# Kernel optimization log

Hardware: AMD Instinct MI355X
Metric: run time of the kernel (lower is better)

The kernel has to match this reference:

```python
import jax, jax.numpy as jnp
import numpy as np

B = 2; D = 256; NH = 8; NL = 4; HD = D // NH
K = 2; P = K * K; NV = 4; DFF = 1024
SHAPES = ((128, 128), (64, 64), (32, 32), (16, 16))
LV = sum(h * w for h, w in SHAPES)
START = np.cumsum([0] + [h * w for h, w in SHAPES])[:-1].tolist()
EPS = 1e-5

# fixed 2x2 sampling kernel, matching _create_kernel_indices (even kernel branch)
_ind = np.linspace(-0.5, 0.5, K)
_ii, _jj = np.meshgrid(_ind, _ind, indexing='ij')
KERNEL = jnp.asarray(np.stack([_jj, _ii], -1).reshape(-1, 2) / K, jnp.float32)  # (P,2)


def _layer_norm(x, w, b):
    m = x.mean(-1, keepdims=True)
    v = ((x - m) ** 2).mean(-1, keepdims=True)
    return (x - m) * jax.lax.rsqrt(v + EPS) * w + b


def _box_attention(query, value, ref_windows, vpw, vpb, opw, opb, boxw, boxb, attw, attb):
    b, lq, _ = query.shape
    # value projection, split into heads: (b, NH, LV, HD)
    v = (value @ vpw.T + vpb).reshape(b, LV, NH, HD).transpose(0, 2, 1, 3)

    # attention weights: softmax over all (level, point) jointly per head
    aw = query @ attw.T + attb
    aw = jax.nn.softmax(aw.reshape(b, lq, NH, NL * P), -1).reshape(b, lq, NH, NL, P)

    # where to attend (with_rotation=False -> 4 offset variables, angle from ref)
    ob = (query @ boxw.T + boxb).reshape(b, lq, NH, NL, NV)
    rw = ref_windows[:, :, None, None, :]                    # (b,lq,1,1,7)
    ref_boxes = rw[..., jnp.array([0, 1, 3, 4])]
    angles = jnp.broadcast_to(rw[..., 6:7], (b, lq, NH, NL, 1))
    boxes = ref_boxes + ob / 8.0 * ref_boxes[..., jnp.array([2, 3, 2, 3])]
    center = boxes[..., None, :2]                            # (b,lq,NH,NL,1,2)
    size = boxes[..., None, 2:]
    c, s = jnp.cos(angles), jnp.sin(angles)
    rot = jnp.stack([c, -s, s, c], -1).reshape(b, lq, NH, NL, 1, 2, 2)
    g = KERNEL * jax.nn.relu(size)                           # (b,lq,NH,NL,P,2)
    grid = center + (g[..., None, :] * rot).sum(-1)          # (b,lq,NH,NL,P,2)

    # multi-level bilinear sampling (= grid_sample align_corners=False, zero pad)
    bidx = jnp.arange(b)[:, None, None, None]
    hidx = jnp.arange(NH)[None, None, :, None]
    out = jnp.zeros((b, lq, NH, HD), v.dtype)
    for lvl, (H, W) in enumerate(SHAPES):
        st = START[lvl]
        vl = v[:, :, st:st + H * W]                          # (b,NH,HW,HD)
        loc = grid[:, :, :, lvl]                             # (b,lq,NH,P,2)
        x = loc[..., 0] * W - 0.5
        y = loc[..., 1] * H - 0.5
        x0f = jnp.floor(x); y0f = jnp.floor(y)
        wx = x - x0f; wy = y - y0f
        x0 = x0f.astype(jnp.int32); y0 = y0f.astype(jnp.int32)
        acc = jnp.zeros((b, lq, NH, P, HD), v.dtype)
        corners = ((0, 0, (1 - wx) * (1 - wy)), (1, 0, wx * (1 - wy)),
                   (0, 1, (1 - wx) * wy), (1, 1, wx * wy))
        for dx, dy, wgt in corners:
            xi = x0 + dx; yi = y0 + dy
            valid = (xi >= 0) & (xi < W) & (yi >= 0) & (yi < H)
            idx = jnp.clip(yi, 0, H - 1) * W + jnp.clip(xi, 0, W - 1)
            samp = vl[bidx, hidx, idx]                       # (b,lq,NH,P,HD)
            acc = acc + (wgt * valid)[..., None] * samp
        out = out + jnp.einsum('blhp,blhpd->blhd', aw[:, :, :, lvl], acc)
    return out.reshape(b, lq, D) @ opw.T + opb


def setup_inputs() -> dict:
    key = jax.random.key(0)
    ks = jax.random.split(key, 20)
    def nrm(k, shape, fan_in):
        return jax.random.normal(k, shape, jnp.float32) * (1.0 / np.sqrt(fan_in))
    rw = jax.random.uniform(ks[2], (B, LV, 7), jnp.float32)
    # keep window sizes (cols 3,4,5) modest, like real BEV reference windows
    rw = rw.at[..., 3:6].multiply(0.2)
    return {
        'src': jax.random.normal(ks[0], (B, LV, D), jnp.float32),
        'pos': jax.random.normal(ks[1], (B, LV, D), jnp.float32),
        'src_shape': jnp.asarray(SHAPES, jnp.int32),
        'src_start_idx': jnp.asarray(START, jnp.int32),
        'ref_windows': rw,
        'vpw': nrm(ks[3], (D, D), D), 'vpb': jnp.zeros((D,), jnp.float32),
        'opw': nrm(ks[4], (D, D), D), 'opb': jnp.zeros((D,), jnp.float32),
        'boxw': nrm(ks[5], (NL * NH * NV, D), D) * 0.1,
        'boxb': jax.random.normal(ks[6], (NL * NH * NV,), jnp.float32) * 0.1,
        'attw': nrm(ks[7], (NH * NL * P, D), D),
        'attb': jnp.zeros((NH * NL * P,), jnp.float32),
        'lin1_w': nrm(ks[8], (DFF, D), D), 'lin1_b': jnp.zeros((DFF,), jnp.float32),
        'lin2_w': nrm(ks[9], (D, DFF), DFF), 'lin2_b': jnp.zeros((D,), jnp.float32),
        'ln1_w': jnp.ones((D,), jnp.float32), 'ln1_b': jnp.zeros((D,), jnp.float32),
        'ln2_w': jnp.ones((D,), jnp.float32), 'ln2_b': jnp.zeros((D,), jnp.float32),
    }


def reference(src, pos, src_shape, src_start_idx, ref_windows,
              vpw, vpb, opw, opb, boxw, boxb, attw, attb,
              lin1_w, lin1_b, lin2_w, lin2_b, ln1_w, ln1_b, ln2_w, ln2_b):
    # level shapes/starts are static (SHAPES/START constants); src_shape /
    # src_start_idx are accepted for signature fidelity.
    src2 = _box_attention(src + pos, src, ref_windows,
                          vpw, vpb, opw, opb, boxw, boxb, attw, attb)
    src = _layer_norm(src + src2, ln1_w, ln1_b)
    ffn = jax.nn.relu(src @ lin1_w.T + lin1_b) @ lin2_w.T + lin2_b
    return _layer_norm(src + ffn, ln2_w, ln2_b)
```

## Files before the change

kernel.cpp:

```cpp
#include <hip/hip_runtime.h>
#include <stdint.h>

typedef unsigned short u16;
typedef __attribute__((ext_vector_type(8))) short short8;
typedef __attribute__((ext_vector_type(4))) float f32x4;

#define D_    256
#define NH_   8
#define HD_   32
#define LV_   21760
#define DFF_  1024
#define EPS_  1e-5f
#define MH_   21760
#define MT_   43520

__device__ __forceinline__ float bf2f(u16 u) {
    union { uint32_t i; float f; } x; x.i = ((uint32_t)u) << 16; return x.f;
}
__device__ __forceinline__ u16 f2bf(float f) {
    union { float f; uint32_t i; } x; x.f = f;
    uint32_t r = x.i + 0x7FFFu + ((x.i >> 16) & 1u);
    return (u16)(r >> 16);
}
__device__ __forceinline__ uint32_t pk2(float a, float b) {
    return (uint32_t)f2bf(a) | ((uint32_t)f2bf(b) << 16);
}
__device__ __forceinline__ float blo(uint32_t u) {
    union { uint32_t i; float f; } x; x.i = u << 16; return x.f;
}
__device__ __forceinline__ float bhi(uint32_t u) {
    union { uint32_t i; float f; } x; x.i = u & 0xffff0000u; return x.f;
}
__device__ __forceinline__ void cv8(u16* dst, float4 a, float4 b) {
    uint4 r;
    r.x = pk2(a.x, a.y); r.y = pk2(a.z, a.w);
    r.z = pk2(b.x, b.y); r.w = pk2(b.z, b.w);
    *(uint4*)dst = r;
}
__device__ __forceinline__ void cv8add(u16* dst, float4 a, float4 a2, float4 b, float4 b2) {
    uint4 r;
    r.x = pk2(a.x + a2.x, a.y + a2.y); r.y = pk2(a.z + a2.z, a.w + a2.w);
    r.z = pk2(b.x + b2.x, b.y + b2.y); r.w = pk2(b.z + b2.z, b.w + b2.w);
    *(uint4*)dst = r;
}

__global__ __launch_bounds__(256) void k_cvt(const float* __restrict__ in,
                                             u16* __restrict__ out, int n4) {
    int i = blockIdx.x * 256 + threadIdx.x;
    if (i < n4) {
        float4 v = ((const float4*)in)[i];
        uint2 r; r.x = pk2(v.x, v.y); r.y = pk2(v.z, v.w);
        *(uint2*)(out + (size_t)i * 4) = r;
    }
}

__global__ __launch_bounds__(256) void k_vprojm(
        const float* __restrict__ src, const float* __restrict__ vpw,
        const float* __restrict__ vpb, u16* __restrict__ vout) {
    __shared__ u16 As[2][64 * 32];
    __shared__ u16 Bs[2][64 * 32];
    const int t = threadIdx.x;
    const int l = t & 63, w = t >> 6;
    const int m0 = blockIdx.x * 64, n0 = blockIdx.y * 64;
    const int sr = t >> 2, sc = t & 3;
    const int wslot = sr * 32 + ((sc ^ ((sr >> 1) & 3)) << 3);
    const float* gA = src + (size_t)(m0 + sr) * 256 + sc * 8;
    const float* gB = vpw + (size_t)(n0 + sr) * 256 + sc * 8;
    const int fr = l & 15, fg = l >> 4;
    const int wm = w >> 1, wn = w & 1;

    f32x4 acc[2][2];
    #pragma unroll
    for (int mi = 0; mi < 2; ++mi)
        #pragma unroll
        for (int ni = 0; ni < 2; ++ni)
            acc[mi][ni] = (f32x4){0.f, 0.f, 0.f, 0.f};

    cv8(&As[0][wslot], *(const float4*)gA, *(const float4*)(gA + 4));
    cv8(&Bs[0][wslot], *(const float4*)gB, *(const float4*)(gB + 4));
    __syncthreads();

    for (int kt = 0; kt < 8; ++kt) {
        const int cur = kt & 1;
        float4 na0, na1, nb0, nb1;
        if (kt < 7) {
            na0 = *(const float4*)(gA + (kt + 1) * 32);
            na1 = *(const float4*)(gA + (kt + 1) * 32 + 4);
            nb0 = *(const float4*)(gB + (kt + 1) * 32);
            nb1 = *(const float4*)(gB + (kt + 1) * 32 + 4);
        }
        short8 af[2], bfr[2];
        #pragma unroll
        for (int mi = 0; mi < 2; ++mi) {
            const int r = wm * 32 + mi * 16 + fr;
            af[mi] = *(const short8*)&As[cur][r * 32 + ((fg ^ ((r >> 1) & 3)) << 3)];
        }
        #pragma unroll
        for (int ni = 0; ni < 2; ++ni) {
            const int r = wn * 32 + ni * 16 + fr;
            bfr[ni] = *(const short8*)&Bs[cur][r * 32 + ((fg ^ ((r >> 1) & 3)) << 3)];
        }
        #pragma unroll
        for (int mi = 0; mi < 2; ++mi)
            #pragma unroll
            for (int ni = 0; ni < 2; ++ni)
                acc[mi][ni] = __builtin_amdgcn_mfma_f32_16x16x32_bf16(af[mi], bfr[ni], acc[mi][ni], 0, 0, 0);
        if (kt < 7) {
            cv8(&As[cur ^ 1][wslot], na0, na1);
            cv8(&Bs[cur ^ 1][wslot], nb0, nb1);
            __syncthreads();
        }
    }
    const int b = m0 / LV_;
    #pragma unroll
    for (int ni = 0; ni < 2; ++ni) {
        const int n = n0 + wn * 32 + ni * 16 + fr;
        const float bv = vpb[n];
        const int h = n >> 5, hd = n & 31;
        #pragma unroll
        for (int mi = 0; mi < 2; ++mi) {
            #pragma unroll
            for (int q = 0; q < 4; ++q) {
                const int m = m0 + wm * 32 + mi * 16 + fg * 4 + q;
                const int lrow = m - b * LV_;
                vout[((size_t)(b * NH_ + h) * LV_ + lrow) * HD_ + hd] = f2bf(acc[mi][ni][q] + bv);
            }
        }
    }
}

__global__ __launch_bounds__(256) void k_logits(
        const float* __restrict__ src, const float* __restrict__ pos,
        const float* __restrict__ attw, const float* __restrict__ attb,
        const float* __restrict__ boxw, const float* __restrict__ boxb,
        u16* __restrict__ lgout) {
    __shared__ u16 As[2][64 * 32];
    __shared__ u16 Bs[2][64 * 32];
    const int t = threadIdx.x;
    const int l = t & 63, w = t >> 6;
    const int m0 = blockIdx.x * 64;
    const int n0g = blockIdx.y * 64;
    const float* Bsrc = (n0g < 128) ? (attw + (size_t)n0g * 256) : (boxw + (size_t)(n0g - 128) * 256);
    const float* bsrc = (n0g < 128) ? (attb + n0g) : (boxb + (n0g - 128));
    const int sr = t >> 2, sc = t & 3;
    const int wslot = sr * 32 + ((sc ^ ((sr >> 1) & 3)) << 3);
    const float* gAs = src + (size_t)(m0 + sr) * 256 + sc * 8;
    const float* gAp = pos + (size_t)(m0 + sr) * 256 + sc * 8;
    const float* gB  = Bsrc + (size_t)sr * 256 + sc * 8;
    const int fr = l & 15, fg = l >> 4;
    const int wm = w >> 1, wn = w & 1;

    f32x4 acc[2][2];
    #pragma unroll
    for (int mi = 0; mi < 2; ++mi)
        #pragma unroll
        for (int ni = 0; ni < 2; ++ni)
            acc[mi][ni] = (f32x4){0.f, 0.f, 0.f, 0.f};

    cv8add(&As[0][wslot], *(const float4*)gAs, *(const float4*)gAp,
                          *(const float4*)(gAs + 4), *(const float4*)(gAp + 4));
    cv8(&Bs[0][wslot], *(const float4*)gB, *(const float4*)(gB + 4));
    __syncthreads();

    for (int kt = 0; kt < 8; ++kt) {
        const int cur = kt & 1;
        float4 ns0, ns1, np0, np1, nb0, nb1;
        if (kt < 7) {
            ns0 = *(const float4*)(gAs + (kt + 1) * 32);
            ns1 = *(const float4*)(gAs + (kt + 1) * 32 + 4);
            np0 = *(const float4*)(gAp + (kt + 1) * 32);
            np1 = *(const float4*)(gAp + (kt + 1) * 32 + 4);
            nb0 = *(const float4*)(gB + (kt + 1) * 32);
            nb1 = *(const float4*)(gB + (kt + 1) * 32 + 4);
        }
        short8 af[2], bfr[2];
        #pragma unroll
        for (int mi = 0; mi < 2; ++mi) {
            const int r = wm * 32 + mi * 16 + fr;
            af[mi] = *(const short8*)&As[cur][r * 32 + ((fg ^ ((r >> 1) & 3)) << 3)];
        }
        #pragma unroll
        for (int ni = 0; ni < 2; ++ni) {
            const int r = wn * 32 + ni * 16 + fr;
            bfr[ni] = *(const short8*)&Bs[cur][r * 32 + ((fg ^ ((r >> 1) & 3)) << 3)];
        }
        #pragma unroll
        for (int mi = 0; mi < 2; ++mi)
            #pragma unroll
            for (int ni = 0; ni < 2; ++ni)
                acc[mi][ni] = __builtin_amdgcn_mfma_f32_16x16x32_bf16(af[mi], bfr[ni], acc[mi][ni], 0, 0, 0);
        if (kt < 7) {
            cv8add(&As[cur ^ 1][wslot], ns0, np0, ns1, np1);
            cv8(&Bs[cur ^ 1][wslot], nb0, nb1);
            __syncthreads();
        }
    }
    #pragma unroll
    for (int ni = 0; ni < 2; ++ni) {
        const int nl_ = wn * 32 + ni * 16 + fr;
        const int n = n0g + nl_;
        const float bv = bsrc[nl_];
        const int off = (n < 128) ? ((n >> 4) * 32 + (n & 15))
                                  : (((n - 128) >> 4) * 32 + 16 + ((n - 128) & 15));
        #pragma unroll
        for (int mi = 0; mi < 2; ++mi) {
            #pragma unroll
            for (int q = 0; q < 4; ++q) {
                const int m = m0 + wm * 32 + mi * 16 + fg * 4 + q;
                lgout[(size_t)m * 256 + off] = f2bf(acc[mi][ni][q] + bv);
            }
        }
    }
}

__global__ __launch_bounds__(256) void k_sample(
        const u16* __restrict__ lg, const float* __restrict__ refw,
        const u16* __restrict__ vws, u16* __restrict__ smp) {
    __shared__ float LG[16][2][32];
    __shared__ float RW[16][8];
    __shared__ __align__(16) uint2 CWI[32 * 66];
    const int t = threadIdx.x;
    const int bid = blockIdx.x;
    const int combo = bid & 7;
    const int idx = bid >> 3;
    const int b = combo >> 2, hp = combo & 3;
    const int h0 = hp * 2;
    const long gr0 = (long)b * LV_ + (long)idx * 16;

    {
        const int row = t >> 4, part = t & 15;
        const uint2 v = *(const uint2*)(lg + (size_t)(gr0 + row) * 256 + h0 * 32 + part * 4);
        const int hs = part >> 3, kk = (part & 7) * 4;
        LG[row][hs][kk]     = blo(v.x);
        LG[row][hs][kk + 1] = bhi(v.x);
        LG[row][hs][kk + 2] = blo(v.y);
        LG[row][hs][kk + 3] = bhi(v.y);
        if (t < 112) {
            int r2 = t / 7, k = t % 7;
            RW[r2][k] = refw[(gr0 + r2) * 7 + k];
        }
    }
    __syncthreads();
    if (t < 32) {
        const int row = t >> 1, hs = t & 1;
        float* a = LG[row][hs];
        float m = a[0];
        #pragma unroll
        for (int k = 1; k < 16; ++k) m = fmaxf(m, a[k]);
        float s = 0.f;
        float e[16];
        #pragma unroll
        for (int k = 0; k < 16; ++k) { e[k] = __expf(a[k] - m); s += e[k]; }
        const float inv = 1.f / s;
        #pragma unroll
        for (int k = 0; k < 16; ++k) a[k] = e[k] * inv;
    }
    __syncthreads();
    #pragma unroll
    for (int uu = 0; uu < 2; ++uu) {
        const int u = t + uu * 256;
        const int row = u >> 5, rem = u & 31;
        const int hs = rem >> 4, nl = (rem >> 2) & 3, p = rem & 3;
        const float rw0 = RW[row][0], rw1 = RW[row][1], rw3 = RW[row][3], rw4 = RW[row][4], ang = RW[row][6];
        const float ob0 = LG[row][hs][16 + nl * 4 + 0];
        const float ob1 = LG[row][hs][16 + nl * 4 + 1];
        const float ob2 = LG[row][hs][16 + nl * 4 + 2];
        const float ob3 = LG[row][hs][16 + nl * 4 + 3];
        const float cx = rw0 + ob0 * 0.125f * rw3;
        const float cy = rw1 + ob1 * 0.125f * rw4;
        const float bw = fmaxf(rw3 + ob2 * 0.125f * rw3, 0.f);
        const float bh = fmaxf(rw4 + ob3 * 0.125f * rw4, 0.f);
        const float kx = (p & 1) ? 0.25f : -0.25f;
        const float ky = (p >> 1) ? 0.25f : -0.25f;
        float sth, cth;
        __sincosf(ang, &sth, &cth);
        const float g0 = kx * bw, g1 = ky * bh;
        const float gx = cx + g0 * cth - g1 * sth;
        const float gy = cy + g0 * sth + g1 * cth;
        const int Wl = 128 >> nl;
        const int st = (65536 - (65536 >> (2 * nl))) / 3;
        const float x = gx * Wl - 0.5f, y = gy * Wl - 0.5f;
        const float xf = floorf(x), yf = floorf(y);
        const float wx = x - xf, wy = y - yf;
        const int x0 = (int)xf, y0 = (int)yf;
        const float awv = LG[row][hs][nl * 4 + p];
        uint2 cw[4];
        #pragma unroll
        for (int c4 = 0; c4 < 4; ++c4) {
            const int dx = c4 & 1, dy = c4 >> 1;
            const int xi = x0 + dx, yi = y0 + dy;
            const float wgt = (dx ? wx : 1.f - wx) * (dy ? wy : 1.f - wy);
            const bool valid = (xi >= 0) && (xi < Wl) && (yi >= 0) && (yi < Wl);
            const int xc = xi < 0 ? 0 : (xi > Wl - 1 ? Wl - 1 : xi);
            const int yc = yi < 0 ? 0 : (yi > Wl - 1 ? Wl - 1 : yi);
            const float wv = valid ? wgt * awv : 0.f;
            cw[c4].x = __float_as_uint(wv);
            cw[c4].y = (uint32_t)(st + yc * Wl + xc) * 64u;
        }
        uint2* dst = &CWI[(row * 2 + hs) * 66 + (nl * 4 + p) * 4];
        *(uint4*)(dst)     = *(const uint4*)&cw[0];
        *(uint4*)(dst + 2) = *(const uint4*)&cw[2];
    }
    __syncthreads();
    {
        const int e = t & 7, g = t >> 3;
        const int row = g >> 1, hs = g & 1, h = h0 + hs;
        const char* vbp = (const char*)vws +
            (((size_t)(b * NH_ + h) * LV_) * HD_ + e * 4) * 2;
        const uint2* cbase = &CWI[g * 66];
        float a0 = 0.f, a1 = 0.f, a2 = 0.f, a3 = 0.f;
        #pragma unroll 4
        for (int k = 0; k < 16; ++k) {
            #pragma unroll
            for (int cc = 0; cc < 2; ++cc) {
                const uint4 cw2 = *(const uint4*)&cbase[k * 4 + cc * 2];
                const float w0 = __uint_as_float(cw2.x);
                const uint2 d0 = *(const uint2*)(vbp + cw2.y);
                const float w1 = __uint_as_float(cw2.z);
                const uint2 d1 = *(const uint2*)(vbp + cw2.w);
                a0 += w0 * blo(d0.x); a1 += w0 * bhi(d0.x);
                a2 += w0 * blo(d0.y); a3 += w0 * bhi(d0.y);
                a0 += w1 * blo(d1.x); a1 += w1 * bhi(d1.x);
                a2 += w1 * blo(d1.y); a3 += w1 * bhi(d1.y);
            }
        }
        uint2 o; o.x = pk2(a0, a1); o.y = pk2(a2, a3);
        *(uint2*)(smp + (size_t)(gr0 + row) * 256 + h * 32 + e * 4) = o;
    }
}

__global__ __launch_bounds__(256) void k_oproj(
        const u16* __restrict__ A,
        const float* __restrict__ opw,
        const float* __restrict__ opb,
        const float* __restrict__ src,
        const float* __restrict__ lnw, const float* __restrict__ lnb,
        u16* __restrict__ out) {
    __shared__ char smem[36864];
    u16* As = (u16*)smem;
    u16* Bs = (u16*)(smem + 4096);
    float* Y = (float*)smem;
    const int t = threadIdx.x;
    const int l = t & 63, w = t >> 6;
    const int m0 = blockIdx.x * 32;
    const int sAr = t >> 2, sc = t & 3;
    const int aslot = sAr * 32 + ((sc ^ ((sAr >> 1) & 3)) << 3);
    const u16* gA = A + (size_t)(m0 + sAr) * 256 + sc * 8;
    const float* gB[4];
    int bslot[4];
    #pragma unroll
    for (int i = 0; i < 4; ++i) {
        const int r = (t >> 2) + i * 64;
        gB[i] = opw + (size_t)r * 256 + sc * 8;
        bslot[i] = r * 32 + ((sc ^ ((r >> 1) & 3)) << 3);
    }
    const int fr = l & 15, fg = l >> 4;

    f32x4 acc[2][4];
    #pragma unroll
    for (int mi = 0; mi < 2; ++mi)
        #pragma unroll
        for (int ni = 0; ni < 4; ++ni)
            acc[mi][ni] = (f32x4){0.f, 0.f, 0.f, 0.f};

    if (t < 128) *(uint4*)&As[aslot] = *(const uint4*)gA;
    #pragma unroll
    for (int i = 0; i < 4; ++i)
        cv8(&Bs[bslot[i]], *(const float4*)gB[i], *(const float4*)(gB[i] + 4));
    __syncthreads();

    for (int kt = 0; kt < 8; ++kt) {
        const int cur = kt & 1;
        uint4 na; float4 nb[4][2];
        if (kt < 7) {
            if (t < 128) na = *(const uint4*)(gA + (kt + 1) * 32);
            #pragma unroll
            for (int i = 0; i < 4; ++i) {
                nb[i][0] = *(const float4*)(gB[i] + (kt + 1) * 32);
                nb[i][1] = *(const float4*)(gB[i] + (kt + 1) * 32 + 4);
            }
        }
        short8 af[2], bfr[4];
        #pragma unroll
        for (int mi = 0; mi < 2; ++mi) {
            const int r = mi * 16 + fr;
            af[mi] = *(const short8*)&As[cur * 1024 + r * 32 + ((fg ^ ((r >> 1) & 3)) << 3)];
        }
        #pragma unroll
        for (int ni = 0; ni < 4; ++ni) {
            const int r = w * 64 + ni * 16 + fr;
            bfr[ni] = *(const short8*)&Bs[cur * 8192 + r * 32 + ((fg ^ ((r >> 1) & 3)) << 3)];
        }
        #pragma unroll
        for (int mi = 0; mi < 2; ++mi)
            #pragma unroll
            for (int ni = 0; ni < 4; ++ni)
                acc[mi][ni] = __builtin_amdgcn_mfma_f32_16x16x32_bf16(af[mi], bfr[ni], acc[mi][ni], 0, 0, 0);
        if (kt < 7) {
            if (t < 128) *(uint4*)&As[(cur ^ 1) * 1024 + aslot] = na;
            #pragma unroll
            for (int i = 0; i < 4; ++i)
                cv8(&Bs[(cur ^ 1) * 8192 + bslot[i]], nb[i][0], nb[i][1]);
            __syncthreads();
        }
    }
    __syncthreads();
    #pragma unroll
    for (int ni = 0; ni < 4; ++ni) {
        const int n = w * 64 + ni * 16 + fr;
        const float bv = opb[n];
        #pragma unroll
        for (int mi = 0; mi < 2; ++mi) {
            #pragma unroll
            for (int q = 0; q < 4; ++q) {
                const int ml = mi * 16 + fg * 4 + q;
                Y[ml * 256 + n] = acc[mi][ni][q] + bv + src[(size_t)(m0 + ml) * 256 + n];
            }
        }
    }
    __syncthreads();
    for (int rr = 0; rr < 8; ++rr) {
        const int m = w * 8 + rr;
        const float v0 = Y[m * 256 + l];
        const float v1 = Y[m * 256 + 64 + l];
        const float v2 = Y[m * 256 + 128 + l];
        const float v3 = Y[m * 256 + 192 + l];
        float s1 = v0 + v1 + v2 + v3;
        float s2 = v0 * v0 + v1 * v1 + v2 * v2 + v3 * v3;
        #pragma unroll
        for (int off = 32; off; off >>= 1) {
            s1 += __shfl_xor(s1, off);
            s2 += __shfl_xor(s2, off);
        }
        const float mean = s1 * (1.f / 256.f);
        const float var = s2 * (1.f / 256.f) - mean * mean;
        const float rs = rsqrtf(var + EPS_);
        const size_t ob = (size_t)(m0 + m) * 256;
        out[ob + l]       = f2bf((v0 - mean) * rs * lnw[l]       + lnb[l]);
        out[ob + 64 + l]  = f2bf((v1 - mean) * rs * lnw[64 + l]  + lnb[64 + l]);
        out[ob + 128 + l] = f2bf((v2 - mean) * rs * lnw[128 + l] + lnb[128 + l]);
        out[ob + 192 + l] = f2bf((v3 - mean) * rs * lnw[192 + l] + lnb[192 + l]);
    }
}

__global__ __launch_bounds__(256) void k_gemm1(
        const u16* __restrict__ A, const u16* __restrict__ Bw,
        const float* __restrict__ bias, u16* __restrict__ H) {
    __shared__ u16 As[2][128 * 32];
    __shared__ u16 Bs[2][128 * 32];
    const int t = threadIdx.x;
    const int l = t & 63, w = t >> 6;
    const int m0 = blockIdx.x * 128, n0 = blockIdx.y * 128;
    const int sr = t >> 1, sc0 = (t & 1) * 2;
    const int ws0 = sr * 32 + ((sc0 ^ ((sr >> 1) & 3)) << 3);
    const int ws1 = sr * 32 + (((sc0 + 1) ^ ((sr >> 1) & 3)) << 3);
    const u16* gA = A + (size_t)(m0 + sr) * 256 + sc0 * 8;
    const u16* gB = Bw + (size_t)(n0 + sr) * 256 + sc0 * 8;
    const int fr = l & 15, fg = l >> 4;
    const int wm = w >> 1, wn = w & 1;

    f32x4 acc[4][4];
    #pragma unroll
    for (int mi = 0; mi < 4; ++mi)
        #pragma unroll
        for (int ni = 0; ni < 4; ++ni)
            acc[mi][ni] = (f32x4){0.f, 0.f, 0.f, 0.f};

    *(uint4*)&As[0][ws0] = *(const uint4*)(gA);
    *(uint4*)&As[0][ws1] = *(const uint4*)(gA + 8);
    *(uint4*)&Bs[0][ws0] = *(const uint4*)(gB);
    *(uint4*)&Bs[0][ws1] = *(const uint4*)(gB + 8);
    __syncthreads();

    for (int kt = 0; kt < 8; ++kt) {
        const int cur = kt & 1;
        uint4 na0, na1, nb0, nb1;
        if (kt < 7) {
            na0 = *(const uint4*)(gA + (kt + 1) * 32);
            na1 = *(const uint4*)(gA + (kt + 1) * 32 + 8);
            nb0 = *(const uint4*)(gB + (kt + 1) * 32);
            nb1 = *(const uint4*)(gB + (kt + 1) * 32 + 8);
        }
        short8 af[4], bfr[4];
        #pragma unroll
        for (int mi = 0; mi < 4; ++mi) {
            const int r = wm * 64 + mi * 16 + fr;
            af[mi] = *(const short8*)&As[cur][r * 32 + ((fg ^ ((r >> 1) & 3)) << 3)];
        }
        #pragma unroll
        for (int ni = 0; ni < 4; ++ni) {
            const int r = wn * 64 + ni * 16 + fr;
            bfr[ni] = *(const short8*)&Bs[cur][r * 32 + ((fg ^ ((r >> 1) & 3)) << 3)];
        }
        #pragma unroll
        for (int mi = 0; mi < 4; ++mi)
            #pragma unroll
            for (int ni = 0; ni < 4; ++ni)
                acc[mi][ni] = __builtin_amdgcn_mfma_f32_16x16x32_bf16(af[mi], bfr[ni], acc[mi][ni], 0, 0, 0);
        if (kt < 7) {
            *(uint4*)&As[cur ^ 1][ws0] = na0;
            *(uint4*)&As[cur ^ 1][ws1] = na1;
            *(uint4*)&Bs[cur ^ 1][ws0] = nb0;
            *(uint4*)&Bs[cur ^ 1][ws1] = nb1;
            __syncthreads();
        }
    }
    #pragma unroll
    for (int ni = 0; ni < 4; ++ni) {
        const int n = n0 + wn * 64 + ni * 16 + fr;
        const float bv = bias[n];
        #pragma unroll
        for (int mi = 0; mi < 4; ++mi) {
            #pragma unroll
            for (int q = 0; q < 4; ++q) {
                const int m = m0 + wm * 64 + mi * 16 + fg * 4 + q;
                const float v = acc[mi][ni][q] + bv;
                H[(size_t)m * 1024 + n] = f2bf(fmaxf(v, 0.f));
            }
        }
    }
}

__global__ __launch_bounds__(256) void k_gemm2(
        const u16* __restrict__ A, const u16* __restrict__ Bw,
        const float* __restrict__ bias, const u16* __restrict__ resid,
        const float* __restrict__ lnw, const float* __restrict__ lnb,
        float* __restrict__ out) {
    __shared__ char smem[36864];
    u16* As = (u16*)smem;
    u16* Bs = (u16*)(smem + 4096);
    float* Y = (float*)smem;
    const int t = threadIdx.x;
    const int l = t & 63, w = t >> 6;
    const int m0 = blockIdx.x * 32;
    const int sAr = t >> 2, sc = t & 3;
    const int aslot = sAr * 32 + ((sc ^ ((sAr >> 1) & 3)) << 3);
    const u16* gA = A + (size_t)(m0 + sAr) * 1024 + sc * 8;
    const u16* gB[4];
    int bslot[4];
    #pragma unroll
    for (int i = 0; i < 4; ++i) {
        const int r = (t >> 2) + i * 64;
        gB[i] = Bw + (size_t)r * 1024 + sc * 8;
        bslot[i] = r * 32 + ((sc ^ ((r >> 1) & 3)) << 3);
    }
    const int fr = l & 15, fg = l >> 4;

    f32x4 acc[2][4];
    #pragma unroll
    for (int mi = 0; mi < 2; ++mi)
        #pragma unroll
        for (int ni = 0; ni < 4; ++ni)
            acc[mi][ni] = (f32x4){0.f, 0.f, 0.f, 0.f};

    if (t < 128) *(uint4*)&As[aslot] = *(const uint4*)(gA);
    #pragma unroll
    for (int i = 0; i < 4; ++i) *(uint4*)&Bs[bslot[i]] = *(const uint4*)(gB[i]);
    __syncthreads();

    for (int kt = 0; kt < 32; ++kt) {
        const int cur = kt & 1;
        uint4 na, nb[4];
        if (kt < 31) {
            if (t < 128) na = *(const uint4*)(gA + (kt + 1) * 32);
            #pragma unroll
            for (int i = 0; i < 4; ++i) nb[i] = *(const uint4*)(gB[i] + (kt + 1) * 32);
        }
        short8 af[2], bfr[4];
        #pragma unroll
        for (int mi = 0; mi < 2; ++mi) {
            const int r = mi * 16 + fr;
            af[mi] = *(const short8*)&As[cur * 1024 + r * 32 + ((fg ^ ((r >> 1) & 3)) << 3)];
        }
        #pragma unroll
        for (int ni = 0; ni < 4; ++ni) {
            const int r = w * 64 + ni * 16 + fr;
            bfr[ni] = *(const short8*)&Bs[cur * 8192 + r * 32 + ((fg ^ ((r >> 1) & 3)) << 3)];
        }
        #pragma unroll
        for (int mi = 0; mi < 2; ++mi)
            #pragma unroll
            for (int ni = 0; ni < 4; ++ni)
                acc[mi][ni] = __builtin_amdgcn_mfma_f32_16x16x32_bf16(af[mi], bfr[ni], acc[mi][ni], 0, 0, 0);
        if (kt < 31) {
            if (t < 128) *(uint4*)&As[(cur ^ 1) * 1024 + aslot] = na;
            #pragma unroll
            for (int i = 0; i < 4; ++i) *(uint4*)&Bs[(cur ^ 1) * 8192 + bslot[i]] = nb[i];
            __syncthreads();
        }
    }
    __syncthreads();
    #pragma unroll
    for (int ni = 0; ni < 4; ++ni) {
        const int n = w * 64 + ni * 16 + fr;
        const float bv = bias[n];
        #pragma unroll
        for (int mi = 0; mi < 2; ++mi) {
            #pragma unroll
            for (int q = 0; q < 4; ++q) {
                const int ml = mi * 16 + fg * 4 + q;
                Y[ml * 256 + n] = acc[mi][ni][q] + bv + bf2f(resid[(size_t)(m0 + ml) * 256 + n]);
            }
        }
    }
    __syncthreads();
    for (int rr = 0; rr < 8; ++rr) {
        const int m = w * 8 + rr;
        const float v0 = Y[m * 256 + l];
        const float v1 = Y[m * 256 + 64 + l];
        const float v2 = Y[m * 256 + 128 + l];
        const float v3 = Y[m * 256 + 192 + l];
        float s1 = v0 + v1 + v2 + v3;
        float s2 = v0 * v0 + v1 * v1 + v2 * v2 + v3 * v3;
        #pragma unroll
        for (int off = 32; off; off >>= 1) {
            s1 += __shfl_xor(s1, off);
            s2 += __shfl_xor(s2, off);
        }
        const float mean = s1 * (1.f / 256.f);
        const float var = s2 * (1.f / 256.f) - mean * mean;
        const float rs = rsqrtf(var + EPS_);
        const size_t ob = (size_t)(m0 + m) * 256;
        out[ob + l]        = (v0 - mean) * rs * lnw[l]        + lnb[l];
        out[ob + 64 + l]   = (v1 - mean) * rs * lnw[64 + l]   + lnb[64 + l];
        out[ob + 128 + l]  = (v2 - mean) * rs * lnw[128 + l]  + lnb[128 + l];
        out[ob + 192 + l]  = (v3 - mean) * rs * lnw[192 + l]  + lnb[192 + l];
    }
}

extern "C" void kernel_launch(void* const* d_in, const int* in_sizes, int n_in,
                              void* d_out, int out_size, void* d_ws, size_t ws_size,
                              hipStream_t stream) {
    const float* src  = (const float*)d_in[0];
    const float* pos  = (const float*)d_in[1];
    const float* refw = (const float*)d_in[4];
    const float* vpw  = (const float*)d_in[5];
    const float* vpb  = (const float*)d_in[6];
    const float* opw  = (const float*)d_in[7];
    const float* opb  = (const float*)d_in[8];
    const float* boxw = (const float*)d_in[9];
    const float* boxb = (const float*)d_in[10];
    const float* attw = (const float*)d_in[11];
    const float* attb = (const float*)d_in[12];
    const float* l1w  = (const float*)d_in[13];
    const float* l1b  = (const float*)d_in[14];
    const float* l2w  = (const float*)d_in[15];
    const float* l2b  = (const float*)d_in[16];
    const float* ln1w = (const float*)d_in[17];
    const float* ln1b = (const float*)d_in[18];
    const float* ln2w = (const float*)d_in[19];
    const float* ln2b = (const float*)d_in[20];

    u16*   vws    = (u16*)d_ws;
    u16*   l1wb   = (u16*)d_ws;
    u16*   l2wb   = (u16*)((char*)d_ws + 524288);
    u16*   logitsb= (u16*)((char*)d_ws + 22282240u);
    u16*   src1b  = (u16*)((char*)d_ws + 22282240u);
    u16*   Hbf    = (u16*)((char*)d_ws + 44564480u);
    u16*   smp    = (u16*)((char*)d_ws + 66846720u);

    hipLaunchKernelGGL(k_vprojm, dim3(680, 4), dim3(256), 0, stream, src, vpw, vpb, vws);
    hipLaunchKernelGGL(k_logits, dim3(680, 4), dim3(256), 0, stream,
                       src, pos, attw, attb, boxw, boxb, logitsb);
    hipLaunchKernelGGL(k_sample, dim3(10880), dim3(256), 0, stream, logitsb, refw, vws, smp);
    hipLaunchKernelGGL(k_cvt, dim3(256), dim3(256), 0, stream, l1w, l1wb, 65536);
    hipLaunchKernelGGL(k_cvt, dim3(256), dim3(256), 0, stream, l2w, l2wb, 65536);
    hipLaunchKernelGGL(k_oproj, dim3(1360), dim3(256), 0, stream,
                       smp, opw, opb, src, ln1w, ln1b, src1b);
    for (int h = 0; h < 2; ++h) {
        const u16* Ah = src1b + (size_t)h * MH_ * 256;
        float* outh   = (float*)d_out + (size_t)h * MH_ * 256;
        hipLaunchKernelGGL(k_gemm1, dim3(170, 8), dim3(256), 0, stream, Ah, l1wb, l1b, Hbf);
        hipLaunchKernelGGL(k_gemm2, dim3(680), dim3(256), 0, stream, Hbf, l2wb, l2b, Ah, ln2w, ln2b, outh);
    }
}
```

Baseline: 320.8 us.

## Double M tiles in projection GEMMs, use hardware bf16 pack, repad sampler LDS

Doubles the M tile of k_vprojm and k_logits to 128 rows and of k_oproj to 64 rows, so each weight tile loaded from global memory and converted is reused across more rows and fewer blocks are launched. Replaces the software round-to-nearest bf16 packing with the v_cvt_pk_bf16_f32 instruction. Changes the k_sample LDS layout with new padding and a precomputed head-plane offset to reduce bank conflicts and address math. k_oproj now stages the pre-LayerNorm residual in LDS as bf16 rather than fp32 to fit the larger tile, which adds rounding before the normalisation statistics and raises register pressure.

```diff
diff --git a/kernel.cpp b/kernel.cpp
--- a/kernel.cpp
+++ b/kernel.cpp
@@ -17,13 +17,13 @@
 __device__ __forceinline__ float bf2f(u16 u) {
     union { uint32_t i; float f; } x; x.i = ((uint32_t)u) << 16; return x.f;
 }
+__device__ __forceinline__ uint32_t pk2(float a, float b) {
+    uint32_t r;
+    asm("v_cvt_pk_bf16_f32 %0, %1, %2" : "=v"(r) : "v"(a), "v"(b));
+    return r;
+}
 __device__ __forceinline__ u16 f2bf(float f) {
-    union { float f; uint32_t i; } x; x.f = f;
-    uint32_t r = x.i + 0x7FFFu + ((x.i >> 16) & 1u);
-    return (u16)(r >> 16);
-}
-__device__ __forceinline__ uint32_t pk2(float a, float b) {
-    return (uint32_t)f2bf(a) | ((uint32_t)f2bf(b) << 16);
+    return (u16)(pk2(f, f) & 0xffffu);
 }
 __device__ __forceinline__ float blo(uint32_t u) {
     union { uint32_t i; float f; } x; x.i = u << 16; return x.f;
@@ -57,42 +57,48 @@
 __global__ __launch_bounds__(256) void k_vprojm(
         const float* __restrict__ src, const float* __restrict__ vpw,
         const float* __restrict__ vpb, u16* __restrict__ vout) {
-    __shared__ u16 As[2][64 * 32];
+    __shared__ u16 As[2][128 * 32];
     __shared__ u16 Bs[2][64 * 32];
     const int t = threadIdx.x;
     const int l = t & 63, w = t >> 6;
-    const int m0 = blockIdx.x * 64, n0 = blockIdx.y * 64;
-    const int sr = t >> 2, sc = t & 3;
-    const int wslot = sr * 32 + ((sc ^ ((sr >> 1) & 3)) << 3);
-    const float* gA = src + (size_t)(m0 + sr) * 256 + sc * 8;
-    const float* gB = vpw + (size_t)(n0 + sr) * 256 + sc * 8;
+    const int m0 = blockIdx.x * 128, n0 = blockIdx.y * 64;
+    const int r0 = t >> 2, c0 = t & 3;
+    const int wsA0 = r0 * 32 + ((c0 ^ ((r0 >> 1) & 3)) << 3);
+    const int wsA1 = wsA0 + 64 * 32;
+    const int wsB  = wsA0;
+    const float* gA0 = src + (size_t)(m0 + r0) * 256 + c0 * 8;
+    const float* gA1 = gA0 + (size_t)64 * 256;
+    const float* gB  = vpw + (size_t)(n0 + r0) * 256 + c0 * 8;
     const int fr = l & 15, fg = l >> 4;
     const int wm = w >> 1, wn = w & 1;
 
-    f32x4 acc[2][2];
-    #pragma unroll
-    for (int mi = 0; mi < 2; ++mi)
+    f32x4 acc[4][2];
+    #pragma unroll
+    for (int mi = 0; mi < 4; ++mi)
         #pragma unroll
         for (int ni = 0; ni < 2; ++ni)
             acc[mi][ni] = (f32x4){0.f, 0.f, 0.f, 0.f};
 
-    cv8(&As[0][wslot], *(const float4*)gA, *(const float4*)(gA + 4));
-    cv8(&Bs[0][wslot], *(const float4*)gB, *(const float4*)(gB + 4));
+    cv8(&As[0][wsA0], *(const float4*)gA0, *(const float4*)(gA0 + 4));
+    cv8(&As[0][wsA1], *(const float4*)gA1, *(const float4*)(gA1 + 4));
+    cv8(&Bs[0][wsB],  *(const float4*)gB,  *(const float4*)(gB + 4));
     __syncthreads();
 
     for (int kt = 0; kt < 8; ++kt) {
         const int cur = kt & 1;
-        float4 na0, na1, nb0, nb1;
-        if (kt < 7) {
-            na0 = *(const float4*)(gA + (kt + 1) * 32);
-            na1 = *(const float4*)(gA + (kt + 1) * 32 + 4);
+        float4 na0, na1, na2, na3, nb0, nb1;
+        if (kt < 7) {
+            na0 = *(const float4*)(gA0 + (kt + 1) * 32);
+            na1 = *(const float4*)(gA0 + (kt + 1) * 32 + 4);
+            na2 = *(const float4*)(gA1 + (kt + 1) * 32);
+            na3 = *(const float4*)(gA1 + (kt + 1) * 32 + 4);
             nb0 = *(const float4*)(gB + (kt + 1) * 32);
             nb1 = *(const float4*)(gB + (kt + 1) * 32 + 4);
         }
-        short8 af[2], bfr[2];
-        #pragma unroll
-        for (int mi = 0; mi < 2; ++mi) {
-            const int r = wm * 32 + mi * 16 + fr;
+        short8 af[4], bfr[2];
+        #pragma unroll
+        for (int mi = 0; mi < 4; ++mi) {
+            const int r = wm * 64 + mi * 16 + fr;
             af[mi] = *(const short8*)&As[cur][r * 32 + ((fg ^ ((r >> 1) & 3)) << 3)];
         }
         #pragma unroll
@@ -101,13 +107,14 @@
             bfr[ni] = *(const short8*)&Bs[cur][r * 32 + ((fg ^ ((r >> 1) & 3)) << 3)];
         }
         #pragma unroll
-        for (int mi = 0; mi < 2; ++mi)
+        for (int mi = 0; mi < 4; ++mi)
             #pragma unroll
             for (int ni = 0; ni < 2; ++ni)
                 acc[mi][ni] = __builtin_amdgcn_mfma_f32_16x16x32_bf16(af[mi], bfr[ni], acc[mi][ni], 0, 0, 0);
         if (kt < 7) {
-            cv8(&As[cur ^ 1][wslot], na0, na1);
-            cv8(&Bs[cur ^ 1][wslot], nb0, nb1);
+            cv8(&As[cur ^ 1][wsA0], na0, na1);
+            cv8(&As[cur ^ 1][wsA1], na2, na3);
+            cv8(&Bs[cur ^ 1][wsB],  nb0, nb1);
             __syncthreads();
         }
     }
@@ -118,10 +125,10 @@
         const float bv = vpb[n];
         const int h = n >> 5, hd = n & 31;
         #pragma unroll
-        for (int mi = 0; mi < 2; ++mi) {
+        for (int mi = 0; mi < 4; ++mi) {
             #pragma unroll
             for (int q = 0; q < 4; ++q) {
-                const int m = m0 + wm * 32 + mi * 16 + fg * 4 + q;
+                const int m = m0 + wm * 64 + mi * 16 + fg * 4 + q;
                 const int lrow = m - b * LV_;
                 vout[((size_t)(b * NH_ + h) * LV_ + lrow) * HD_ + hd] = f2bf(acc[mi][ni][q] + bv);
             }
@@ -134,49 +141,59 @@
         const float* __restrict__ attw, const float* __restrict__ attb,
         const float* __restrict__ boxw, const float* __restrict__ boxb,
         u16* __restrict__ lgout) {
-    __shared__ u16 As[2][64 * 32];
+    __shared__ u16 As[2][128 * 32];
     __shared__ u16 Bs[2][64 * 32];
     const int t = threadIdx.x;
     const int l = t & 63, w = t >> 6;
-    const int m0 = blockIdx.x * 64;
+    const int m0 = blockIdx.x * 128;
     const int n0g = blockIdx.y * 64;
     const float* Bsrc = (n0g < 128) ? (attw + (size_t)n0g * 256) : (boxw + (size_t)(n0g - 128) * 256);
     const float* bsrc = (n0g < 128) ? (attb + n0g) : (boxb + (n0g - 128));
-    const int sr = t >> 2, sc = t & 3;
-    const int wslot = sr * 32 + ((sc ^ ((sr >> 1) & 3)) << 3);
-    const float* gAs = src + (size_t)(m0 + sr) * 256 + sc * 8;
-    const float* gAp = pos + (size_t)(m0 + sr) * 256 + sc * 8;
-    const float* gB  = Bsrc + (size_t)sr * 256 + sc * 8;
+    const int r0 = t >> 2, c0 = t & 3;
+    const int wsA0 = r0 * 32 + ((c0 ^ ((r0 >> 1) & 3)) << 3);
+    const int wsA1 = wsA0 + 64 * 32;
+    const int wsB  = wsA0;
+    const float* gAs0 = src + (size_t)(m0 + r0) * 256 + c0 * 8;
+    const float* gAp0 = pos + (size_t)(m0 + r0) * 256 + c0 * 8;
+    const float* gAs1 = gAs0 + (size_t)64 * 256;
+    const float* gAp1 = gAp0 + (size_t)64 * 256;
+    const float* gB   = Bsrc + (size_t)r0 * 256 + c0 * 8;
     const int fr = l & 15, fg = l >> 4;
     const int wm = w >> 1, wn = w & 1;
 
-    f32x4 acc[2][2];
-    #pragma unroll
-    for (int mi = 0; mi < 2; ++mi)
+    f32x4 acc[4][2];
+    #pragma unroll
+    for (int mi = 0; mi < 4; ++mi)
         #pragma unroll
         for (int ni = 0; ni < 2; ++ni)
             acc[mi][ni] = (f32x4){0.f, 0.f, 0.f, 0.f};
 
-    cv8add(&As[0][wslot], *(const float4*)gAs, *(const float4*)gAp,
-                          *(const float4*)(gAs + 4), *(const float4*)(gAp + 4));
-    cv8(&Bs[0][wslot], *(const float4*)gB, *(const float4*)(gB + 4));
+    cv8add(&As[0][wsA0], *(const float4*)gAs0, *(const float4*)gAp0,
+                         *(const float4*)(gAs0 + 4), *(const float4*)(gAp0 + 4));
+    cv8add(&As[0][wsA1], *(const float4*)gAs1, *(const float4*)gAp1,
+                         *(const float4*)(gAs1 + 4), *(const float4*)(gAp1 + 4));
+    cv8(&Bs[0][wsB], *(const float4*)gB, *(const float4*)(gB + 4));
     __syncthreads();
 
     for (int kt = 0; kt < 8; ++kt) {
         const int cur = kt & 1;
-        float4 ns0, ns1, np0, np1, nb0, nb1;
-        if (kt < 7) {
-            ns0 = *(const float4*)(gAs + (kt + 1) * 32);
-            ns1 = *(const float4*)(gAs + (kt + 1) * 32 + 4);
-            np0 = *(const float4*)(gAp + (kt + 1) * 32);
-            np1 = *(const float4*)(gAp + (kt + 1) * 32 + 4);
+        float4 ns0, ns1, np0, np1, ns2, ns3, np2, np3, nb0, nb1;
+        if (kt < 7) {
+            ns0 = *(const float4*)(gAs0 + (kt + 1) * 32);
+            ns1 = *(const float4*)(gAs0 + (kt + 1) * 32 + 4);
+            np0 = *(const float4*)(gAp0 + (kt + 1) * 32);
+            np1 = *(const float4*)(gAp0 + (kt + 1) * 32 + 4);
+            ns2 = *(const float4*)(gAs1 + (kt + 1) * 32);
+            ns3 = *(const float4*)(gAs1 + (kt + 1) * 32 + 4);
+            np2 = *(const float4*)(gAp1 + (kt + 1) * 32);
+            np3 = *(const float4*)(gAp1 + (kt + 1) * 32 + 4);
             nb0 = *(const float4*)(gB + (kt + 1) * 32);
             nb1 = *(const float4*)(gB + (kt + 1) * 32 + 4);
         }
-        short8 af[2], bfr[2];
-        #pragma unroll
-        for (int mi = 0; mi < 2; ++mi) {
-            const int r = wm * 32 + mi * 16 + fr;
+        short8 af[4], bfr[2];
+        #pragma unroll
+        for (int mi = 0; mi < 4; ++mi) {
+            const int r = wm * 64 + mi * 16 + fr;
             af[mi] = *(const short8*)&As[cur][r * 32 + ((fg ^ ((r >> 1) & 3)) << 3)];
         }
         #pragma unroll
@@ -185,13 +202,14 @@
             bfr[ni] = *(const short8*)&Bs[cur][r * 32 + ((fg ^ ((r >> 1) & 3)) << 3)];
         }
         #pragma unroll
-        for (int mi = 0; mi < 2; ++mi)
+        for (int mi = 0; mi < 4; ++mi)
             #pragma unroll
             for (int ni = 0; ni < 2; ++ni)
                 acc[mi][ni] = __builtin_amdgcn_mfma_f32_16x16x32_bf16(af[mi], bfr[ni], acc[mi][ni], 0, 0, 0);
         if (kt < 7) {
-            cv8add(&As[cur ^ 1][wslot], ns0, np0, ns1, np1);
-            cv8(&Bs[cur ^ 1][wslot], nb0, nb1);
+            cv8add(&As[cur ^ 1][wsA0], ns0, np0, ns1, np1);
+            cv8add(&As[cur ^ 1][wsA1], ns2, np2, ns3, np3);
+            cv8(&Bs[cur ^ 1][wsB], nb0, nb1);
             __syncthreads();
         }
     }
@@ -203,10 +221,10 @@
         const int off = (n < 128) ? ((n >> 4) * 32 + (n & 15))
                                   : (((n - 128) >> 4) * 32 + 16 + ((n - 128) & 15));
         #pragma unroll
-        for (int mi = 0; mi < 2; ++mi) {
+        for (int mi = 0; mi < 4; ++mi) {
             #pragma unroll
             for (int q = 0; q < 4; ++q) {
-                const int m = m0 + wm * 32 + mi * 16 + fg * 4 + q;
+                const int m = m0 + wm * 64 + mi * 16 + fg * 4 + q;
                 lgout[(size_t)m * 256 + off] = f2bf(acc[mi][ni][q] + bv);
             }
         }
@@ -216,9 +234,9 @@
 __global__ __launch_bounds__(256) void k_sample(
         const u16* __restrict__ lg, const float* __restrict__ refw,
         const u16* __restrict__ vws, u16* __restrict__ smp) {
-    __shared__ float LG[16][2][32];
+    __shared__ float LG[16][2][36];
     __shared__ float RW[16][8];
-    __shared__ __align__(16) uint2 CWI[32 * 66];
+    __shared__ __align__(16) uint2 CWI[32 * 68];
     const int t = threadIdx.x;
     const int bid = blockIdx.x;
     const int combo = bid & 7;
@@ -226,6 +244,7 @@
     const int b = combo >> 2, hp = combo & 3;
     const int h0 = hp * 2;
     const long gr0 = (long)b * LV_ + (long)idx * 16;
+    const uint32_t PLANEB = (uint32_t)LV_ * HD_ * 2;
 
     {
         const int row = t >> 4, part = t & 15;
@@ -284,6 +303,7 @@
         const float wx = x - xf, wy = y - yf;
         const int x0 = (int)xf, y0 = (int)yf;
         const float awv = LG[row][hs][nl * 4 + p];
+        const uint32_t hoff = hs ? PLANEB : 0u;
         uint2 cw[4];
         #pragma unroll
         for (int c4 = 0; c4 < 4; ++c4) {
@@ -295,25 +315,26 @@
             const int yc = yi < 0 ? 0 : (yi > Wl - 1 ? Wl - 1 : yi);
             const float wv = valid ? wgt * awv : 0.f;
             cw[c4].x = __float_as_uint(wv);
-            cw[c4].y = (uint32_t)(st + yc * Wl + xc) * 64u;
-        }
-        uint2* dst = &CWI[(row * 2 + hs) * 66 + (nl * 4 + p) * 4];
-        *(uint4*)(dst)     = *(const uint4*)&cw[0];
-        *(uint4*)(dst + 2) = *(const uint4*)&cw[2];
+            cw[c4].y = (uint32_t)(st + yc * Wl + xc) * 64u + hoff;
+        }
+        const int g = row * 2 + hs, un = nl * 4 + p;
+        uint2* d0 = &CWI[g * 68 + un * 2];
+        *(uint4*)(d0)      = *(const uint4*)&cw[0];
+        *(uint4*)(d0 + 34) = *(const uint4*)&cw[2];
     }
     __syncthreads();
     {
         const int e = t & 7, g = t >> 3;
-        const int row = g >> 1, hs = g & 1, h = h0 + hs;
+        const int row = g >> 1, hs = g & 1;
         const char* vbp = (const char*)vws +
-            (((size_t)(b * NH_ + h) * LV_) * HD_ + e * 4) * 2;
-        const uint2* cbase = &CWI[g * 66];
+            (((size_t)(b * NH_ + h0) * LV_) * HD_ + e * 4) * 2;
+        const uint2* cbase = &CWI[g * 68];
         float a0 = 0.f, a1 = 0.f, a2 = 0.f, a3 = 0.f;
         #pragma unroll 4
         for (int k = 0; k < 16; ++k) {
             #pragma unroll
             for (int cc = 0; cc < 2; ++cc) {
-                const uint4 cw2 = *(const uint4*)&cbase[k * 4 + cc * 2];
+                const uint4 cw2 = *(const uint4*)&cbase[cc * 34 + k * 2];
                 const float w0 = __uint_as_float(cw2.x);
                 const uint2 d0 = *(const uint2*)(vbp + cw2.y);
                 const float w1 = __uint_as_float(cw2.z);
@@ -325,7 +346,7 @@
             }
         }
         uint2 o; o.x = pk2(a0, a1); o.y = pk2(a2, a3);
-        *(uint2*)(smp + (size_t)(gr0 + row) * 256 + h * 32 + e * 4) = o;
+        *(uint2*)(smp + (size_t)(gr0 + row) * 256 + (h0 + hs) * 32 + e * 4) = o;
     }
 }
 
@@ -336,34 +357,34 @@
         const float* __restrict__ src,
         const float* __restrict__ lnw, const float* __restrict__ lnb,
         u16* __restrict__ out) {
-    __shared__ char smem[36864];
+    __shared__ char smem[40960];
     u16* As = (u16*)smem;
-    u16* Bs = (u16*)(smem + 4096);
-    float* Y = (float*)smem;
+    u16* Bs = (u16*)(smem + 8192);
+    u16* Y  = (u16*)smem;
     const int t = threadIdx.x;
     const int l = t & 63, w = t >> 6;
-    const int m0 = blockIdx.x * 32;
-    const int sAr = t >> 2, sc = t & 3;
-    const int aslot = sAr * 32 + ((sc ^ ((sAr >> 1) & 3)) << 3);
-    const u16* gA = A + (size_t)(m0 + sAr) * 256 + sc * 8;
+    const int m0 = blockIdx.x * 64;
+    const int r0 = t >> 2, sc = t & 3;
+    const int aslot = r0 * 32 + ((sc ^ ((r0 >> 1) & 3)) << 3);
+    const u16* gA = A + (size_t)(m0 + r0) * 256 + sc * 8;
     const float* gB[4];
     int bslot[4];
     #pragma unroll
     for (int i = 0; i < 4; ++i) {
-        const int r = (t >> 2) + i * 64;
+        const int r = r0 + i * 64;
         gB[i] = opw + (size_t)r * 256 + sc * 8;
         bslot[i] = r * 32 + ((sc ^ ((r >> 1) & 3)) << 3);
     }
     const int fr = l & 15, fg = l >> 4;
 
-    f32x4 acc[2][4];
-    #pragma unroll
-    for (int mi = 0; mi < 2; ++mi)
+    f32x4 acc[4][4];
+    #pragma unroll
+    for (int mi = 0; mi < 4; ++mi)
         #pragma unroll
         for (int ni = 0; ni < 4; ++ni)
             acc[mi][ni] = (f32x4){0.f, 0.f, 0.f, 0.f};
 
-    if (t < 128) *(uint4*)&As[aslot] = *(const uint4*)gA;
+    *(uint4*)&As[aslot] = *(const uint4*)gA;
     #pragma unroll
     for (int i = 0; i < 4; ++i)
         cv8(&Bs[bslot[i]], *(const float4*)gB[i], *(const float4*)(gB[i] + 4));
@@ -373,18 +394,18 @@
         const int cur = kt & 1;
         uint4 na; float4 nb[4][2];
         if (kt < 7) {
-            if (t < 128) na = *(const uint4*)(gA + (kt + 1) * 32);
+            na = *(const uint4*)(gA + (kt + 1) * 32);
             #pragma unroll
             for (int i = 0; i < 4; ++i) {
                 nb[i][0] = *(const float4*)(gB[i] + (kt + 1) * 32);
                 nb[i][1] = *(const float4*)(gB[i] + (kt + 1) * 32 + 4);
             }
         }
-        short8 af[2], bfr[4];
-        #pragma unroll
-        for (int mi = 0; mi < 2; ++mi) {
+        short8 af[4], bfr[4];
+        #pragma unroll
+        for (int mi = 0; mi < 4; ++mi) {
             const int r = mi * 16 + fr;
-            af[mi] = *(const short8*)&As[cur * 1024 + r * 32 + ((fg ^ ((r >> 1) & 3)) << 3)];
+            af[mi] = *(const short8*)&As[cur * 2048 + r * 32 + ((fg ^ ((r >> 1) & 3)) << 3)];
         }
         #pragma unroll
         for (int ni = 0; ni < 4; ++ni) {
@@ -392,12 +413,12 @@
             bfr[ni] = *(const short8*)&Bs[cur * 8192 + r * 32 + ((fg ^ ((r >> 1) & 3)) << 3)];
         }
         #pragma unroll
-        for (int mi = 0; mi < 2; ++mi)
+        for (int mi = 0; mi < 4; ++mi)
             #pragma unroll
             for (int ni = 0; ni < 4; ++ni)
                 acc[mi][ni] = __builtin_amdgcn_mfma_f32_16x16x32_bf16(af[mi], bfr[ni], acc[mi][ni], 0, 0, 0);
         if (kt < 7) {
-            if (t < 128) *(uint4*)&As[(cur ^ 1) * 1024 + aslot] = na;
+            *(uint4*)&As[(cur ^ 1) * 2048 + aslot] = na;
             #pragma unroll
             for (int i = 0; i < 4; ++i)
                 cv8(&Bs[(cur ^ 1) * 8192 + bslot[i]], nb[i][0], nb[i][1]);
@@ -410,21 +431,21 @@
         const int n = w * 64 + ni * 16 + fr;
         const float bv = opb[n];
         #pragma unroll
-        for (int mi = 0; mi < 2; ++mi) {
+        for (int mi = 0; mi < 4; ++mi) {
             #pragma unroll
             for (int q = 0; q < 4; ++q) {
                 const int ml = mi * 16 + fg * 4 + q;
-                Y[ml * 256 + n] = acc[mi][ni][q] + bv + src[(size_t)(m0 + ml) * 256 + n];
+                Y[ml * 256 + n] = f2bf(acc[mi][ni][q] + bv + src[(size_t)(m0 + ml) * 256 + n]);
             }
         }
     }
     __syncthreads();
-    for (int rr = 0; rr < 8; ++rr) {
-        const int m = w * 8 + rr;
-        const float v0 = Y[m * 256 + l];
-        const float v1 = Y[m * 256 + 64 + l];
-        const float v2 = Y[m * 256 + 128 + l];
-        const float v3 = Y[m * 256 + 192 + l];
+    for (int rr = 0; rr < 16; ++rr) {
+        const int m = w * 16 + rr;
+        const float v0 = bf2f(Y[m * 256 + l]);
+        const float v1 = bf2f(Y[m * 256 + 64 + l]);
+        const float v2 = bf2f(Y[m * 256 + 128 + l]);
+        const float v3 = bf2f(Y[m * 256 + 192 + l]);
         float s1 = v0 + v1 + v2 + v3;
         float s2 = v0 * v0 + v1 * v1 + v2 * v2 + v3 * v3;
         #pragma unroll
@@ -659,13 +680,13 @@
     u16*   Hbf    = (u16*)((char*)d_ws + 44564480u);
     u16*   smp    = (u16*)((char*)d_ws + 66846720u);
 
-    hipLaunchKernelGGL(k_vprojm, dim3(680, 4), dim3(256), 0, stream, src, vpw, vpb, vws);
-    hipLaunchKernelGGL(k_logits, dim3(680, 4), dim3(256), 0, stream,
+    hipLaunchKernelGGL(k_vprojm, dim3(340, 4), dim3(256), 0, stream, src, vpw, vpb, vws);
+    hipLaunchKernelGGL(k_logits, dim3(340, 4), dim3(256), 0, stream,
                        src, pos, attw, attb, boxw, boxb, logitsb);
     hipLaunchKernelGGL(k_sample, dim3(10880), dim3(256), 0, stream, logitsb, refw, vws, smp);
     hipLaunchKernelGGL(k_cvt, dim3(256), dim3(256), 0, stream, l1w, l1wb, 65536);
     hipLaunchKernelGGL(k_cvt, dim3(256), dim3(256), 0, stream, l2w, l2wb, 65536);
-    hipLaunchKernelGGL(k_oproj, dim3(1360), dim3(256), 0, stream,
+    hipLaunchKernelGGL(k_oproj, dim3(680), dim3(256), 0, stream,
                        smp, opw, opb, src, ln1w, ln1b, src1b);
     for (int h = 0; h < 2; ++h) {
         const u16* Ah = src1b + (size_t)h * MH_ * 256;
```

Result: slower. 338.3 us (+5.5%).
